# Performance work log

Measured on AMD Instinct MI355X. Metric: run time of the kernel, lower is better.

Reference implementation:

```python
import jax, jax.numpy as jnp
import numpy as np

B, T, D, H, L, O = 256, 512, 64, 256, 2, 4


def _lstm_layer(x_tbd, W_ih, W_hh, b_ih, b_hh):
    """x_tbd: (T, B, D_in) -> hidden sequence (T, B, H). PyTorch gate order i,f,g,o."""
    Bb = x_tbd.shape[1]
    Hh = W_hh.shape[1]
    b = b_ih + b_hh
    # precompute input projections for all timesteps in one GEMM
    xW = jnp.einsum('tbd,gd->tbg', x_tbd, W_ih) + b  # (T, B, 4H)

    def step(carry, xw_t):
        h, c = carry
        gates = xw_t + h @ W_hh.T
        i, f, g, o = jnp.split(gates, 4, axis=-1)
        i = jax.nn.sigmoid(i)
        f = jax.nn.sigmoid(f)
        g = jnp.tanh(g)
        o = jax.nn.sigmoid(o)
        c = f * c + i * g
        h = o * jnp.tanh(c)
        return (h, c), h

    init = (jnp.zeros((Bb, Hh), x_tbd.dtype), jnp.zeros((Bb, Hh), x_tbd.dtype))
    _, hs = jax.lax.scan(step, init, xW)
    return hs


def setup_inputs() -> dict:
    key = jax.random.key(0)
    ks = jax.random.split(key, 11)
    s = 1.0 / np.sqrt(H)  # PyTorch LSTM init scale
    inp = {
        'x': jax.random.normal(ks[0], (B, T, D), dtype=jnp.float32),
        'W_ih0': jax.random.uniform(ks[1], (4 * H, D), minval=-s, maxval=s, dtype=jnp.float32),
        'W_hh0': jax.random.uniform(ks[2], (4 * H, H), minval=-s, maxval=s, dtype=jnp.float32),
        'b_ih0': jax.random.uniform(ks[3], (4 * H,), minval=-s, maxval=s, dtype=jnp.float32),
        'b_hh0': jax.random.uniform(ks[4], (4 * H,), minval=-s, maxval=s, dtype=jnp.float32),
        'W_ih1': jax.random.uniform(ks[5], (4 * H, H), minval=-s, maxval=s, dtype=jnp.float32),
        'W_hh1': jax.random.uniform(ks[6], (4 * H, H), minval=-s, maxval=s, dtype=jnp.float32),
        'b_ih1': jax.random.uniform(ks[7], (4 * H,), minval=-s, maxval=s, dtype=jnp.float32),
        'b_hh1': jax.random.uniform(ks[8], (4 * H,), minval=-s, maxval=s, dtype=jnp.float32),
        'fc_W': jax.random.uniform(ks[9], (O, H), minval=-s, maxval=s, dtype=jnp.float32),
        'fc_b': jax.random.uniform(ks[10], (O,), minval=-s, maxval=s, dtype=jnp.float32),
    }
    return inp


def reference(x, W_ih0, W_hh0, b_ih0, b_hh0, W_ih1, W_hh1, b_ih1, b_hh1, fc_W, fc_b):
    xt = jnp.transpose(x, (1, 0, 2))            # (T, B, D), batch_first -> time-major
    h1 = _lstm_layer(xt, W_ih0, W_hh0, b_ih0, b_hh0)   # (T, B, H)
    h2 = _lstm_layer(h1, W_ih1, W_hh1, b_ih1, b_hh1)   # (T, B, H)
    last = h2[-1]                                # out[:, -1, :] in batch_first layout
    return last @ fc_W.T + fc_b                  # (B, O)
```

## Files before the change

### kernel.cpp

```cpp
#include <hip/hip_runtime.h>


#define TT 512
#define HH 256
#define DD 64

typedef __attribute__((ext_vector_type(2))) _Float16 h2t;
typedef __attribute__((ext_vector_type(8))) _Float16 f16x8;
typedef __attribute__((ext_vector_type(4))) float f32x4;
typedef unsigned long long u64;
typedef unsigned u32;

__device__ __forceinline__ u32 pkh(float x, float y) {
    h2t h; h.x = (_Float16)x; h.y = (_Float16)y;
    return __builtin_bit_cast(u32, h);
}
__device__ __forceinline__ float sigf(float x) { return 1.f / (1.f + __expf(-x)); }
__device__ __forceinline__ float tanhf_(float x) {
    float e = __expf(2.f * x);
    return 1.f - 2.f / (e + 1.f);
}
__device__ __forceinline__ f16x8 ld8(const float* p) {
    float4 u = ((const float4*)p)[0];
    float4 v = ((const float4*)p)[1];
    f16x8 r = {(_Float16)u.x, (_Float16)u.y, (_Float16)u.z, (_Float16)u.w,
               (_Float16)v.x, (_Float16)v.y, (_Float16)v.z, (_Float16)v.w};
    return r;
}
__device__ __forceinline__ u32 ld32(const u32* p) {
    return __hip_atomic_load(p, __ATOMIC_RELAXED, __HIP_MEMORY_SCOPE_AGENT);
}
__device__ __forceinline__ void st32(u32* p, u32 v) {
    __hip_atomic_store(p, v, __ATOMIC_RELAXED, __HIP_MEMORY_SCOPE_AGENT);
}
__device__ __forceinline__ u64 ld64(const u64* p) {
    return __hip_atomic_load(p, __ATOMIC_RELAXED, __HIP_MEMORY_SCOPE_AGENT);
}
__device__ __forceinline__ void st64(u64* p, u64 v) {
    __hip_atomic_store(p, v, __ATOMIC_RELAXED, __HIP_MEMORY_SCOPE_AGENT);
}

__global__ __launch_bounds__(512, 2) void lstm_persist(
    const float* __restrict__ x,
    const float* __restrict__ Wih0, const float* __restrict__ Whh0,
    const float* __restrict__ bih0, const float* __restrict__ bhh0,
    const float* __restrict__ Wih1, const float* __restrict__ Whh1,
    const float* __restrict__ bih1, const float* __restrict__ bhh1,
    const float* __restrict__ fcW, const float* __restrict__ fcb,
    float* __restrict__ out,
    u64* h0ring, u64* h1ring, u32* cflagsA)
{
    __shared__ __align__(16) _Float16 sB[9216];
    __shared__ __align__(16) float part2[2][8][276];

    const int tid  = threadIdx.x;
    const int g    = blockIdx.x & 31;
    const int role = blockIdx.x >> 5;
    const bool isL1 = role >= 4;
    const int q = role & 3;
    const int batch0 = g * 8;
    u64* ring0 = h0ring + (size_t)g * 4096;
    u64* ring1 = h1ring + (size_t)g * 4096;
    u32* cflag = cflagsA + (size_t)g * 16;

    const int lane = tid & 63, w = tid >> 6;
    const int mw = w & 3, kh = w >> 2;
    const int bcol = lane & 15, kc = lane >> 4;

    const int R0 = mw * 256 + 64 * q + (lane & 15);
    const int R1 = R0 + 16, R2 = R0 + 32, R3 = R0 + 48;

#define DECL_TI(ti) f16x8 A##ti##_0={},A##ti##_1={},A##ti##_2={},A##ti##_3={}, \
                          A##ti##_4={},A##ti##_5={},A##ti##_6={},A##ti##_7={};
    DECL_TI(0) DECL_TI(1) DECL_TI(2) DECL_TI(3)
#undef DECL_TI

    if (isL1) {
#define LDA1(ti,j) { int k_ = (kh*8+(j))*32 + kc*8;                          \
        A##ti##_##j = ld8(k_ < 256 ? Wih1 + (size_t)R##ti*256 + k_           \
                                   : Whh1 + (size_t)R##ti*256 + (k_-256)); }
#define LDA1T(ti) LDA1(ti,0) LDA1(ti,1) LDA1(ti,2) LDA1(ti,3) \
                  LDA1(ti,4) LDA1(ti,5) LDA1(ti,6) LDA1(ti,7)
        LDA1T(0) LDA1T(1) LDA1T(2) LDA1T(3)
#undef LDA1T
#undef LDA1
    } else {
#define LDA0(ti,j) { int k_ = (kh*5+(j))*32 + kc*8;                          \
        A##ti##_##j = ld8(k_ < 64 ? Wih0 + (size_t)R##ti*64 + k_             \
                                  : Whh0 + (size_t)R##ti*256 + (k_-64)); }
#define LDA0T(ti) LDA0(ti,0) LDA0(ti,1) LDA0(ti,2) LDA0(ti,3) LDA0(ti,4)
        LDA0T(0) LDA0T(1) LDA0T(2) LDA0T(3)
#undef LDA0T
#undef LDA0
    }

    const float* bA = isL1 ? bih1 : bih0;
    const float* bB = isL1 ? bhh1 : bhh0;
    const float bz0 = bA[      64*q + lane] + bB[      64*q + lane];
    const float bz1 = bA[256 + 64*q + lane] + bB[256 + 64*q + lane];
    const float bz2 = bA[512 + 64*q + lane] + bB[512 + 64*q + lane];
    const float bz3 = bA[768 + 64*q + lane] + bB[768 + 64*q + lane];
    float cst = 0.f;

    u32* const sBu = (u32*)sB;
    for (int i = tid; i < 4608; i += 512) sBu[i] = 0;
    __syncthreads();

    if (!isL1 && tid >= 256 && tid < 384) {
        int t2 = tid - 256, j = t2 >> 4, c = t2 & 15;
        float4 v = ((const float4*)(x + ((size_t)(batch0 + j) * TT) * DD))[c];
        int bidx = (c >> 1) * 72 + j * 4 + 2 * (c & 1);
        sBu[bidx]     = pkh(v.x, v.y);
        sBu[bidx + 1] = pkh(v.z, v.w);
    }

    for (int s = 0; s <= TT; ++s) {
        __syncthreads();
        if (tid == 0) st32(&cflag[role], (u32)(s + 1));

        const bool act_ = isL1 ? (s >= 1) : (s < TT);
        const int  snx  = s + 1;
        const bool stg0 = (!isL1) && (snx < TT);
        const bool stg1 = isL1 && (snx <= TT);

        u32 cpre = 0u;
        if (act_ && lane < 8) cpre = ld32(&cflag[lane]);
        float4 xr;
        const bool doX = stg0 && (tid >= 256) && (tid < 384);
        if (doX) {
            int t2 = tid - 256, j = t2 >> 4, c = t2 & 15;
            xr = ((const float4*)(x + ((size_t)(batch0 + j) * TT + snx) * DD))[c];
        }

        if (act_) {
            f32x4 C0 = {0,0,0,0}, C1 = {0,0,0,0}, C2 = {0,0,0,0}, C3 = {0,0,0,0};
#define MST(j, ktb) { const f16x8 Bf = *(const f16x8*)(sB + (((ktb)+(j))*4 + kc)*144 + bcol*8); \
            C0 = __builtin_amdgcn_mfma_f32_16x16x32_f16(A0_##j, Bf, C0, 0,0,0); \
            C1 = __builtin_amdgcn_mfma_f32_16x16x32_f16(A1_##j, Bf, C1, 0,0,0); \
            C2 = __builtin_amdgcn_mfma_f32_16x16x32_f16(A2_##j, Bf, C2, 0,0,0); \
            C3 = __builtin_amdgcn_mfma_f32_16x16x32_f16(A3_##j, Bf, C3, 0,0,0); }
            if (isL1) {
                const int ktb = kh * 8;
                MST(0,ktb) MST(1,ktb) MST(2,ktb) MST(3,ktb)
                MST(4,ktb) MST(5,ktb) MST(6,ktb) MST(7,ktb)
            } else {
                const int ktb = kh * 5;
                MST(0,ktb) MST(1,ktb) MST(2,ktb) MST(3,ktb) MST(4,ktb)
            }
#undef MST
            if (bcol < 8) {
                *(f32x4*)&part2[kh][bcol][mw*64 +  0 + kc*4] = C0;
                *(f32x4*)&part2[kh][bcol][mw*64 + 16 + kc*4] = C1;
                *(f32x4*)&part2[kh][bcol][mw*64 + 32 + kc*4] = C2;
                *(f32x4*)&part2[kh][bcol][mw*64 + 48 + kc*4] = C3;
            }
        }
        __syncthreads();

        if (act_) {
            float s0 = part2[0][w][      lane] + part2[1][w][      lane] + bz0;
            float s1 = part2[0][w][ 64 + lane] + part2[1][w][ 64 + lane] + bz1;
            float s2 = part2[0][w][128 + lane] + part2[1][w][128 + lane] + bz2;
            float s3 = part2[0][w][192 + lane] + part2[1][w][192 + lane] + bz3;
            float fi = sigf(s0), ff = sigf(s1), fg = tanhf_(s2), fo = sigf(s3);
            cst = ff * cst + fi * fg;
            float h = fo * tanhf_(cst);
            float hn = __shfl_down(h, 1);
            u32 hw = pkh(h, hn);

            const int tgt = s - 2;
            while (!__all(lane >= 8 || (int)cpre >= tgt)) {
                __builtin_amdgcn_s_sleep(1);
                if (lane < 8) cpre = ld32(&cflag[lane]);
            }
            if (!(lane & 1)) {
                u64 v = ((u64)(u32)(s + 1) << 32) | (u64)hw;
                u64* dst = (isL1 ? ring1 + (size_t)((s - 1) & 3) * 1024
                                 : ring0 + (size_t)(s & 3) * 1024)
                           + q * 256 + w * 32 + (lane >> 1);
                st64(dst, v);
            }
        }

        if (stg0 || stg1) {
            const int n0  = tid & 127;
            const int jj0 = tid >> 7, jj1 = 4 + jj0;
            const u64* b0 = ring0 + (size_t)((snx - 1) & 3) * 1024
                            + ((n0 >> 5) << 8) + (n0 & 31);
            const u64* a00 = b0 + jj0 * 32;
            const u64* a01 = b0 + jj1 * 32;
            u64 v00, v01, v10 = 0, v11 = 0;
            const u64 *a10 = nullptr, *a11 = nullptr;
            if (isL1) {
                const u64* b1 = ring1 + (size_t)((snx + 2) & 3) * 1024
                                + ((n0 >> 5) << 8) + (n0 & 31);
                a10 = b1 + jj0 * 32; a11 = b1 + jj1 * 32;
                v00 = ld64(a00); v01 = ld64(a01);
                v10 = ld64(a10); v11 = ld64(a11);
            } else {
                v00 = ld64(a00); v01 = ld64(a01);
            }
            const u32 e0 = (u32)snx;
            const u32 e1 = (snx >= 2) ? (u32)snx : 0u;
            for (;;) {
                bool k0 = ((u32)(v00 >> 32) == e0);
                bool k1 = ((u32)(v01 >> 32) == e0);
                bool k2 = !isL1 || ((u32)(v10 >> 32) == e1);
                bool k3 = !isL1 || ((u32)(v11 >> 32) == e1);
                if (k0 & k1 & k2 & k3) break;
                if (!k0) v00 = ld64(a00);
                if (!k1) v01 = ld64(a01);
                if (isL1) {
                    if (!k2) v10 = ld64(a10);
                    if (!k3) v11 = ld64(a11);
                }
            }
            const int cb0 = isL1 ? 0 : 8;
            sBu[(cb0 + (n0 >> 2)) * 72 + jj0 * 4 + (n0 & 3)] = (u32)v00;
            sBu[(cb0 + (n0 >> 2)) * 72 + jj1 * 4 + (n0 & 3)] = (u32)v01;
            if (isL1) {
                sBu[(32 + (n0 >> 2)) * 72 + jj0 * 4 + (n0 & 3)] = (u32)v10;
                sBu[(32 + (n0 >> 2)) * 72 + jj1 * 4 + (n0 & 3)] = (u32)v11;
            }
            if (doX) {
                int t2 = tid - 256, j = t2 >> 4, c = t2 & 15;
                int bidx = (c >> 1) * 72 + j * 4 + 2 * (c & 1);
                sBu[bidx]     = pkh(xr.x, xr.y);
                sBu[bidx + 1] = pkh(xr.z, xr.w);
            }
        }
    }

    if (isL1 && q == 0) {
        const u32 ef = (u32)(TT + 1);
        const int n0  = tid & 127;
        const int jj0 = tid >> 7, jj1 = 4 + jj0;
        const u64* b = ring1 + 3 * 1024 + ((n0 >> 5) << 8) + (n0 & 31);
        const u64* a0 = b + jj0 * 32;
        const u64* a1 = b + jj1 * 32;
        u64 v0 = ld64(a0), v1 = ld64(a1);
        for (;;) {
            bool k0 = ((u32)(v0 >> 32) == ef), k1 = ((u32)(v1 >> 32) == ef);
            if (k0 & k1) break;
            if (!k0) v0 = ld64(a0);
            if (!k1) v1 = ld64(a1);
        }
        sBu[jj0 * 128 + n0] = (u32)v0;
        sBu[jj1 * 128 + n0] = (u32)v1;
        __syncthreads();
        const int j = tid >> 6, l2 = tid & 63;
        const int o = l2 >> 4, kk = l2 & 15;
        float ssum = 0.f;
#pragma unroll
        for (int m = 0; m < 16; ++m) {
            int k = kk * 16 + m;
            ssum += (float)sB[j * 256 + k] * fcW[o * HH + k];
        }
#pragma unroll
        for (int off = 8; off; off >>= 1) ssum += __shfl_down(ssum, off);
        if (kk == 0) out[(batch0 + j) * 4 + o] = ssum + fcb[o];
    }
}

extern "C" void kernel_launch(void* const* d_in, const int* in_sizes, int n_in,
                              void* d_out, int out_size, void* d_ws, size_t ws_size,
                              hipStream_t stream)
{
    (void)in_sizes; (void)n_in; (void)out_size; (void)ws_size;
    const float* x    = (const float*)d_in[0];
    const float* Wih0 = (const float*)d_in[1];
    const float* Whh0 = (const float*)d_in[2];
    const float* bih0 = (const float*)d_in[3];
    const float* bhh0 = (const float*)d_in[4];
    const float* Wih1 = (const float*)d_in[5];
    const float* Whh1 = (const float*)d_in[6];
    const float* bih1 = (const float*)d_in[7];
    const float* bhh1 = (const float*)d_in[8];
    const float* fcW  = (const float*)d_in[9];
    const float* fcb  = (const float*)d_in[10];
    float* out = (float*)d_out;

    u64* h0ring = (u64*)d_ws;
    u64* h1ring = (u64*)((char*)d_ws + 1048576);
    u32* cflags = (u32*)((char*)d_ws + 2097152);

    hipMemsetAsync(d_ws, 0, 2097152 + 2048, stream);

    lstm_persist<<<dim3(256), dim3(512), 0, stream>>>(
        x, Wih0, Whh0, bih0, bhh0, Wih1, Whh1, bih1, bhh1, fcW, fcb, out,
        h0ring, h1ring, cflags);
}
```

Baseline: 1.319 ms.

## Add dedicated loader wave with double-buffered LDS and flag-based intra-block sync

Adds a ninth wavefront per block that polls the global h rings and x, then stages the next step's B operand into a double-buffered LDS tile. The eight compute waves no longer do this staging; they coordinate with the loader and with each other through LDS atomic counters and flags instead of __syncthreads. The goal is to overlap cross-block communication latency with the MFMA and activation work. The cost is 576-thread blocks, with launch bounds no longer requesting 2 blocks per CU, twice the LDS, and spin-wait polling that carries ordering and deadlock risk.

```diff
diff --git a/kernel.cpp b/kernel.cpp
--- a/kernel.cpp
+++ b/kernel.cpp
@@ -39,8 +39,20 @@
 __device__ __forceinline__ void st64(u64* p, u64 v) {
     __hip_atomic_store(p, v, __ATOMIC_RELAXED, __HIP_MEMORY_SCOPE_AGENT);
 }
-
-__global__ __launch_bounds__(512, 2) void lstm_persist(
+__device__ __forceinline__ int ldsLd(const int* p) {
+    return __hip_atomic_load(p, __ATOMIC_ACQUIRE, __HIP_MEMORY_SCOPE_WORKGROUP);
+}
+__device__ __forceinline__ void ldsAdd(int* p) {
+    __hip_atomic_fetch_add(p, 1, __ATOMIC_ACQ_REL, __HIP_MEMORY_SCOPE_WORKGROUP);
+}
+__device__ __forceinline__ void ldsStRel(int* p, int v) {
+    __hip_atomic_store(p, v, __ATOMIC_RELEASE, __HIP_MEMORY_SCOPE_WORKGROUP);
+}
+
+#define R16(M) M(0) M(1) M(2) M(3) M(4) M(5) M(6) M(7) \
+               M(8) M(9) M(10) M(11) M(12) M(13) M(14) M(15)
+
+__global__ __launch_bounds__(576) void lstm_persist(
     const float* __restrict__ x,
     const float* __restrict__ Wih0, const float* __restrict__ Whh0,
     const float* __restrict__ bih0, const float* __restrict__ bhh0,
@@ -50,8 +62,10 @@
     float* __restrict__ out,
     u64* h0ring, u64* h1ring, u32* cflagsA)
 {
-    __shared__ __align__(16) _Float16 sB[9216];
+    __shared__ __align__(16) _Float16 sB[2][9216];
     __shared__ __align__(16) float part2[2][8][276];
+    __shared__ int sFlag[2];
+    __shared__ int mfmaCnt, actCnt;
 
     const int tid  = threadIdx.x;
     const int g    = blockIdx.x & 31;
@@ -63,202 +77,226 @@
     u64* ring1 = h1ring + (size_t)g * 4096;
     u32* cflag = cflagsA + (size_t)g * 16;
 
-    const int lane = tid & 63, w = tid >> 6;
-    const int mw = w & 3, kh = w >> 2;
-    const int bcol = lane & 15, kc = lane >> 4;
-
-    const int R0 = mw * 256 + 64 * q + (lane & 15);
-    const int R1 = R0 + 16, R2 = R0 + 32, R3 = R0 + 48;
+    u32* const sBu = (u32*)&sB[0][0];
+    for (int i = tid; i < 9216; i += 576) sBu[i] = 0;
+    if (tid == 0) { sFlag[0] = -1; sFlag[1] = -1; mfmaCnt = 0; actCnt = 0; }
+    __syncthreads();
+
+    if (tid < 512) {
+        const int lane = tid & 63, w = tid >> 6;
+        const int mw = w & 3, kh = w >> 2;
+        const int bcol = lane & 15, kc = lane >> 4;
+
+        const int R0 = mw * 256 + 64 * q + (lane & 15);
+        const int R1 = R0 + 16, R2 = R0 + 32, R3 = R0 + 48;
 
 #define DECL_TI(ti) f16x8 A##ti##_0={},A##ti##_1={},A##ti##_2={},A##ti##_3={}, \
                           A##ti##_4={},A##ti##_5={},A##ti##_6={},A##ti##_7={};
-    DECL_TI(0) DECL_TI(1) DECL_TI(2) DECL_TI(3)
+        DECL_TI(0) DECL_TI(1) DECL_TI(2) DECL_TI(3)
 #undef DECL_TI
-
-    if (isL1) {
+        if (isL1) {
 #define LDA1(ti,j) { int k_ = (kh*8+(j))*32 + kc*8;                          \
-        A##ti##_##j = ld8(k_ < 256 ? Wih1 + (size_t)R##ti*256 + k_           \
-                                   : Whh1 + (size_t)R##ti*256 + (k_-256)); }
+            A##ti##_##j = ld8(k_ < 256 ? Wih1 + (size_t)R##ti*256 + k_       \
+                                       : Whh1 + (size_t)R##ti*256 + (k_-256)); }
 #define LDA1T(ti) LDA1(ti,0) LDA1(ti,1) LDA1(ti,2) LDA1(ti,3) \
                   LDA1(ti,4) LDA1(ti,5) LDA1(ti,6) LDA1(ti,7)
-        LDA1T(0) LDA1T(1) LDA1T(2) LDA1T(3)
+            LDA1T(0) LDA1T(1) LDA1T(2) LDA1T(3)
 #undef LDA1T
 #undef LDA1
-    } else {
+        } else {
 #define LDA0(ti,j) { int k_ = (kh*5+(j))*32 + kc*8;                          \
-        A##ti##_##j = ld8(k_ < 64 ? Wih0 + (size_t)R##ti*64 + k_             \
-                                  : Whh0 + (size_t)R##ti*256 + (k_-64)); }
+            A##ti##_##j = ld8(k_ < 64 ? Wih0 + (size_t)R##ti*64 + k_         \
+                                      : Whh0 + (size_t)R##ti*256 + (k_-64)); }
 #define LDA0T(ti) LDA0(ti,0) LDA0(ti,1) LDA0(ti,2) LDA0(ti,3) LDA0(ti,4)
-        LDA0T(0) LDA0T(1) LDA0T(2) LDA0T(3)
+            LDA0T(0) LDA0T(1) LDA0T(2) LDA0T(3)
 #undef LDA0T
 #undef LDA0
-    }
-
-    const float* bA = isL1 ? bih1 : bih0;
-    const float* bB = isL1 ? bhh1 : bhh0;
-    const float bz0 = bA[      64*q + lane] + bB[      64*q + lane];
-    const float bz1 = bA[256 + 64*q + lane] + bB[256 + 64*q + lane];
-    const float bz2 = bA[512 + 64*q + lane] + bB[512 + 64*q + lane];
-    const float bz3 = bA[768 + 64*q + lane] + bB[768 + 64*q + lane];
-    float cst = 0.f;
-
-    u32* const sBu = (u32*)sB;
-    for (int i = tid; i < 4608; i += 512) sBu[i] = 0;
-    __syncthreads();
-
-    if (!isL1 && tid >= 256 && tid < 384) {
-        int t2 = tid - 256, j = t2 >> 4, c = t2 & 15;
-        float4 v = ((const float4*)(x + ((size_t)(batch0 + j) * TT) * DD))[c];
-        int bidx = (c >> 1) * 72 + j * 4 + 2 * (c & 1);
-        sBu[bidx]     = pkh(v.x, v.y);
-        sBu[bidx + 1] = pkh(v.z, v.w);
-    }
-
-    for (int s = 0; s <= TT; ++s) {
-        __syncthreads();
-        if (tid == 0) st32(&cflag[role], (u32)(s + 1));
-
-        const bool act_ = isL1 ? (s >= 1) : (s < TT);
-        const int  snx  = s + 1;
-        const bool stg0 = (!isL1) && (snx < TT);
-        const bool stg1 = isL1 && (snx <= TT);
-
-        u32 cpre = 0u;
-        if (act_ && lane < 8) cpre = ld32(&cflag[lane]);
-        float4 xr;
-        const bool doX = stg0 && (tid >= 256) && (tid < 384);
-        if (doX) {
-            int t2 = tid - 256, j = t2 >> 4, c = t2 & 15;
-            xr = ((const float4*)(x + ((size_t)(batch0 + j) * TT + snx) * DD))[c];
-        }
-
-        if (act_) {
+        }
+
+        const float* bA = isL1 ? bih1 : bih0;
+        const float* bB = isL1 ? bhh1 : bhh0;
+        const float bz0 = bA[      64*q + lane] + bB[      64*q + lane];
+        const float bz1 = bA[256 + 64*q + lane] + bB[256 + 64*q + lane];
+        const float bz2 = bA[512 + 64*q + lane] + bB[512 + 64*q + lane];
+        const float bz3 = bA[768 + 64*q + lane] + bB[768 + 64*q + lane];
+        float cst = 0.f;
+
+#define MST(j, ktb) { const f16x8 Bf = *(const f16x8*)(sBp + (((ktb)+(j))*4 + kc)*144 + bcol*8); \
+        C0 = __builtin_amdgcn_mfma_f32_16x16x32_f16(A0_##j, Bf, C0, 0,0,0); \
+        C1 = __builtin_amdgcn_mfma_f32_16x16x32_f16(A1_##j, Bf, C1, 0,0,0); \
+        C2 = __builtin_amdgcn_mfma_f32_16x16x32_f16(A2_##j, Bf, C2, 0,0,0); \
+        C3 = __builtin_amdgcn_mfma_f32_16x16x32_f16(A3_##j, Bf, C3, 0,0,0); }
+
+        for (int s = 0; s <= TT; ++s) {
+            const int par = s & 1;
+            const bool act_ = isL1 ? (s >= 1) : (s < TT);
+
+            if (act_) {
+                while (ldsLd(&sFlag[par]) < s) __builtin_amdgcn_s_sleep(1);
+            }
             f32x4 C0 = {0,0,0,0}, C1 = {0,0,0,0}, C2 = {0,0,0,0}, C3 = {0,0,0,0};
-#define MST(j, ktb) { const f16x8 Bf = *(const f16x8*)(sB + (((ktb)+(j))*4 + kc)*144 + bcol*8); \
-            C0 = __builtin_amdgcn_mfma_f32_16x16x32_f16(A0_##j, Bf, C0, 0,0,0); \
-            C1 = __builtin_amdgcn_mfma_f32_16x16x32_f16(A1_##j, Bf, C1, 0,0,0); \
-            C2 = __builtin_amdgcn_mfma_f32_16x16x32_f16(A2_##j, Bf, C2, 0,0,0); \
-            C3 = __builtin_amdgcn_mfma_f32_16x16x32_f16(A3_##j, Bf, C3, 0,0,0); }
-            if (isL1) {
-                const int ktb = kh * 8;
-                MST(0,ktb) MST(1,ktb) MST(2,ktb) MST(3,ktb)
-                MST(4,ktb) MST(5,ktb) MST(6,ktb) MST(7,ktb)
-            } else {
-                const int ktb = kh * 5;
-                MST(0,ktb) MST(1,ktb) MST(2,ktb) MST(3,ktb) MST(4,ktb)
-            }
-#undef MST
-            if (bcol < 8) {
+            if (act_) {
+                const _Float16* sBp = &sB[par][0];
+                if (isL1) {
+                    const int ktb = kh * 8;
+                    MST(0,ktb) MST(1,ktb) MST(2,ktb) MST(3,ktb)
+                    MST(4,ktb) MST(5,ktb) MST(6,ktb) MST(7,ktb)
+                } else {
+                    const int ktb = kh * 5;
+                    MST(0,ktb) MST(1,ktb) MST(2,ktb) MST(3,ktb) MST(4,ktb)
+                }
+            }
+            u32 cpre = 0u;
+            if (act_ && lane < 8) cpre = ld32(&cflag[lane]);
+
+            while (ldsLd(&actCnt) < 8 * s) __builtin_amdgcn_s_sleep(1);
+            if (act_ && bcol < 8) {
                 *(f32x4*)&part2[kh][bcol][mw*64 +  0 + kc*4] = C0;
                 *(f32x4*)&part2[kh][bcol][mw*64 + 16 + kc*4] = C1;
                 *(f32x4*)&part2[kh][bcol][mw*64 + 32 + kc*4] = C2;
                 *(f32x4*)&part2[kh][bcol][mw*64 + 48 + kc*4] = C3;
             }
-        }
-        __syncthreads();
-
-        if (act_) {
-            float s0 = part2[0][w][      lane] + part2[1][w][      lane] + bz0;
-            float s1 = part2[0][w][ 64 + lane] + part2[1][w][ 64 + lane] + bz1;
-            float s2 = part2[0][w][128 + lane] + part2[1][w][128 + lane] + bz2;
-            float s3 = part2[0][w][192 + lane] + part2[1][w][192 + lane] + bz3;
-            float fi = sigf(s0), ff = sigf(s1), fg = tanhf_(s2), fo = sigf(s3);
-            cst = ff * cst + fi * fg;
-            float h = fo * tanhf_(cst);
-            float hn = __shfl_down(h, 1);
-            u32 hw = pkh(h, hn);
-
-            const int tgt = s - 2;
-            while (!__all(lane >= 8 || (int)cpre >= tgt)) {
-                __builtin_amdgcn_s_sleep(1);
-                if (lane < 8) cpre = ld32(&cflag[lane]);
-            }
-            if (!(lane & 1)) {
-                u64 v = ((u64)(u32)(s + 1) << 32) | (u64)hw;
-                u64* dst = (isL1 ? ring1 + (size_t)((s - 1) & 3) * 1024
-                                 : ring0 + (size_t)(s & 3) * 1024)
-                           + q * 256 + w * 32 + (lane >> 1);
-                st64(dst, v);
-            }
-        }
-
-        if (stg0 || stg1) {
+            if (lane == 0) ldsAdd(&mfmaCnt);
+            while (ldsLd(&mfmaCnt) < 8 * (s + 1)) __builtin_amdgcn_s_sleep(1);
+
+            if (act_) {
+                float s0 = part2[0][w][      lane] + part2[1][w][      lane] + bz0;
+                float s1 = part2[0][w][ 64 + lane] + part2[1][w][ 64 + lane] + bz1;
+                float s2 = part2[0][w][128 + lane] + part2[1][w][128 + lane] + bz2;
+                float s3 = part2[0][w][192 + lane] + part2[1][w][192 + lane] + bz3;
+                float fi = sigf(s0), ff = sigf(s1), fg = tanhf_(s2), fo = sigf(s3);
+                cst = ff * cst + fi * fg;
+                float h = fo * tanhf_(cst);
+                float hn = __shfl_down(h, 1);
+                u32 hw = pkh(h, hn);
+
+                const int tgt = s - 2;
+                while (!__all(lane >= 8 || (int)cpre >= tgt)) {
+                    __builtin_amdgcn_s_sleep(1);
+                    if (lane < 8) cpre = ld32(&cflag[lane]);
+                }
+                if (!(lane & 1)) {
+                    u64 v = ((u64)(u32)(s + 1) << 32) | (u64)hw;
+                    u64* dst = (isL1 ? ring1 + (size_t)((s - 1) & 3) * 1024
+                                     : ring0 + (size_t)(s & 3) * 1024)
+                               + q * 256 + w * 32 + (lane >> 1);
+                    st64(dst, v);
+                }
+            }
+            if (lane == 0) ldsAdd(&actCnt);
+        }
+#undef MST
+    } else {
+        const int l = tid - 512;
+        const int tmin = isL1 ? 1 : 0;
+        const int tmax = isL1 ? TT : TT - 1;
+        for (int t = tmin; t <= tmax; ++t) {
+            if (t >= 2) {
+                while (ldsLd(&mfmaCnt) < 8 * (t - 1)) __builtin_amdgcn_s_sleep(1);
+            }
+            u32* dst = sBu + (t & 1) * 4608;
+            const u64* b0 = ring0 + (size_t)((t - 1) & 3) * 1024;
+            const u32 e0 = (u32)t;
+#define LD0(r) u64 va##r = ld64(b0 + (r) * 64 + l);
+            R16(LD0)
+#undef LD0
+            if (isL1) {
+                const u64* b1 = ring1 + (size_t)((t - 2) & 3) * 1024;
+                const u32 e1 = (t >= 2) ? (u32)t : 0u;
+#define LD1(r) u64 vb##r = ld64(b1 + (r) * 64 + l);
+                R16(LD1)
+#undef LD1
+                u32 remA = 0xFFFFu, remB = 0xFFFFu;
+                for (;;) {
+#define TRYA(r) if ((remA >> (r)) & 1) { if ((u32)(va##r >> 32) == e0) {            \
+                    int idx = (r) * 64 + l;                                          \
+                    int q_ = idx >> 8, j_ = (idx >> 5) & 7;                          \
+                    int n_ = 32 * q_ + (idx & 31);                                   \
+                    dst[(0 + (n_ >> 2)) * 72 + j_ * 4 + (n_ & 3)] = (u32)va##r;      \
+                    remA &= ~(1u << (r)); } }
+                    R16(TRYA)
+#undef TRYA
+#define TRYB(r) if ((remB >> (r)) & 1) { if ((u32)(vb##r >> 32) == e1) {            \
+                    int idx = (r) * 64 + l;                                          \
+                    int q_ = idx >> 8, j_ = (idx >> 5) & 7;                          \
+                    int n_ = 32 * q_ + (idx & 31);                                   \
+                    dst[(32 + (n_ >> 2)) * 72 + j_ * 4 + (n_ & 3)] = (u32)vb##r;     \
+                    remB &= ~(1u << (r)); } }
+                    R16(TRYB)
+#undef TRYB
+                    if (!(remA | remB)) break;
+#define RLA(r) if ((remA >> (r)) & 1) va##r = ld64(b0 + (r) * 64 + l);
+                    R16(RLA)
+#undef RLA
+#define RLB(r) if ((remB >> (r)) & 1) vb##r = ld64(ring1 + (size_t)((t-2)&3)*1024 + (r)*64 + l);
+                    R16(RLB)
+#undef RLB
+                }
+            } else {
+                const int j = l >> 3, c8 = l & 7;
+                const float4* xrow = (const float4*)(
+                    x + ((size_t)(batch0 + j) * TT + t) * DD);
+                float4 xa = xrow[2 * c8], xb = xrow[2 * c8 + 1];
+                u32 remA = 0xFFFFu;
+                for (;;) {
+#define TRYA(r) if ((remA >> (r)) & 1) { if ((u32)(va##r >> 32) == e0) {            \
+                    int idx = (r) * 64 + l;                                          \
+                    int q_ = idx >> 8, j_ = (idx >> 5) & 7;                          \
+                    int n_ = 32 * q_ + (idx & 31);                                   \
+                    dst[(8 + (n_ >> 2)) * 72 + j_ * 4 + (n_ & 3)] = (u32)va##r;      \
+                    remA &= ~(1u << (r)); } }
+                    R16(TRYA)
+#undef TRYA
+                    if (!remA) break;
+#define RLA(r) if ((remA >> (r)) & 1) va##r = ld64(b0 + (r) * 64 + l);
+                    R16(RLA)
+#undef RLA
+                }
+                const int xb0 = c8 * 72 + j * 4;
+                dst[xb0]     = pkh(xa.x, xa.y);
+                dst[xb0 + 1] = pkh(xa.z, xa.w);
+                dst[xb0 + 2] = pkh(xb.x, xb.y);
+                dst[xb0 + 3] = pkh(xb.z, xb.w);
+            }
+            ldsStRel(&sFlag[t & 1], t);
+            st32(&cflag[role], (u32)(t + 1));
+        }
+    }
+    __syncthreads();
+
+    if (isL1 && q == 0) {
+        if (tid < 512) {
+            const u32 ef = (u32)(TT + 1);
             const int n0  = tid & 127;
             const int jj0 = tid >> 7, jj1 = 4 + jj0;
-            const u64* b0 = ring0 + (size_t)((snx - 1) & 3) * 1024
-                            + ((n0 >> 5) << 8) + (n0 & 31);
-            const u64* a00 = b0 + jj0 * 32;
-            const u64* a01 = b0 + jj1 * 32;
-            u64 v00, v01, v10 = 0, v11 = 0;
-            const u64 *a10 = nullptr, *a11 = nullptr;
-            if (isL1) {
-                const u64* b1 = ring1 + (size_t)((snx + 2) & 3) * 1024
-                                + ((n0 >> 5) << 8) + (n0 & 31);
-                a10 = b1 + jj0 * 32; a11 = b1 + jj1 * 32;
-                v00 = ld64(a00); v01 = ld64(a01);
-                v10 = ld64(a10); v11 = ld64(a11);
-            } else {
-                v00 = ld64(a00); v01 = ld64(a01);
-            }
-            const u32 e0 = (u32)snx;
-            const u32 e1 = (snx >= 2) ? (u32)snx : 0u;
+            const u64* b = ring1 + 3 * 1024 + ((size_t)(n0 >> 5) << 8) + (n0 & 31);
+            const u64* a0 = b + jj0 * 32;
+            const u64* a1 = b + jj1 * 32;
+            u64 v0 = ld64(a0), v1 = ld64(a1);
             for (;;) {
-                bool k0 = ((u32)(v00 >> 32) == e0);
-                bool k1 = ((u32)(v01 >> 32) == e0);
-                bool k2 = !isL1 || ((u32)(v10 >> 32) == e1);
-                bool k3 = !isL1 || ((u32)(v11 >> 32) == e1);
-                if (k0 & k1 & k2 & k3) break;
-                if (!k0) v00 = ld64(a00);
-                if (!k1) v01 = ld64(a01);
-                if (isL1) {
-                    if (!k2) v10 = ld64(a10);
-                    if (!k3) v11 = ld64(a11);
-                }
-            }
-            const int cb0 = isL1 ? 0 : 8;
-            sBu[(cb0 + (n0 >> 2)) * 72 + jj0 * 4 + (n0 & 3)] = (u32)v00;
-            sBu[(cb0 + (n0 >> 2)) * 72 + jj1 * 4 + (n0 & 3)] = (u32)v01;
-            if (isL1) {
-                sBu[(32 + (n0 >> 2)) * 72 + jj0 * 4 + (n0 & 3)] = (u32)v10;
-                sBu[(32 + (n0 >> 2)) * 72 + jj1 * 4 + (n0 & 3)] = (u32)v11;
-            }
-            if (doX) {
-                int t2 = tid - 256, j = t2 >> 4, c = t2 & 15;
-                int bidx = (c >> 1) * 72 + j * 4 + 2 * (c & 1);
-                sBu[bidx]     = pkh(xr.x, xr.y);
-                sBu[bidx + 1] = pkh(xr.z, xr.w);
-            }
-        }
-    }
-
-    if (isL1 && q == 0) {
-        const u32 ef = (u32)(TT + 1);
-        const int n0  = tid & 127;
-        const int jj0 = tid >> 7, jj1 = 4 + jj0;
-        const u64* b = ring1 + 3 * 1024 + ((n0 >> 5) << 8) + (n0 & 31);
-        const u64* a0 = b + jj0 * 32;
-        const u64* a1 = b + jj1 * 32;
-        u64 v0 = ld64(a0), v1 = ld64(a1);
-        for (;;) {
-            bool k0 = ((u32)(v0 >> 32) == ef), k1 = ((u32)(v1 >> 32) == ef);
-            if (k0 & k1) break;
-            if (!k0) v0 = ld64(a0);
-            if (!k1) v1 = ld64(a1);
-        }
-        sBu[jj0 * 128 + n0] = (u32)v0;
-        sBu[jj1 * 128 + n0] = (u32)v1;
+                bool k0 = ((u32)(v0 >> 32) == ef), k1 = ((u32)(v1 >> 32) == ef);
+                if (k0 & k1) break;
+                if (!k0) v0 = ld64(a0);
+                if (!k1) v1 = ld64(a1);
+            }
+            sBu[jj0 * 128 + n0] = (u32)v0;
+            sBu[jj1 * 128 + n0] = (u32)v1;
+        }
         __syncthreads();
-        const int j = tid >> 6, l2 = tid & 63;
-        const int o = l2 >> 4, kk = l2 & 15;
-        float ssum = 0.f;
+        if (tid < 512) {
+            const int j = tid >> 6, l2 = tid & 63;
+            const int o = l2 >> 4, kk = l2 & 15;
+            const _Float16* hs = &sB[0][0];
+            float ssum = 0.f;
 #pragma unroll
-        for (int m = 0; m < 16; ++m) {
-            int k = kk * 16 + m;
-            ssum += (float)sB[j * 256 + k] * fcW[o * HH + k];
-        }
+            for (int m = 0; m < 16; ++m) {
+                int k = kk * 16 + m;
+                ssum += (float)hs[j * 256 + k] * fcW[o * HH + k];
+            }
 #pragma unroll
-        for (int off = 8; off; off >>= 1) ssum += __shfl_down(ssum, off);
-        if (kk == 0) out[(batch0 + j) * 4 + o] = ssum + fcb[o];
+            for (int off = 8; off; off >>= 1) ssum += __shfl_down(ssum, off);
+            if (kk == 0) out[(batch0 + j) * 4 + o] = ssum + fcb[o];
+        }
     }
 }
 
@@ -286,7 +324,7 @@
 
     hipMemsetAsync(d_ws, 0, 2097152 + 2048, stream);
 
-    lstm_persist<<<dim3(256), dim3(512), 0, stream>>>(
+    lstm_persist<<<dim3(256), dim3(576), 0, stream>>>(
         x, Wih0, Whh0, bih0, bhh0, Wih1, Whh1, bih1, bhh1, fcW, fcb, out,
         h0ring, h1ring, cflags);
 }
```

Measured after the change: 2.727 ms. 2.07x slower.
